# Performance work log

Measured on AMD Instinct MI355X. Metric: run time of the kernel, lower is better.

The kernel has to match this reference:

```python
import jax, jax.numpy as jnp
import numpy as np

EMBED_DIM = 1024
NUM_HEADS = 16
DEPTH = EMBED_DIM // NUM_HEADS
B, S = 4, 2048


def setup_inputs() -> dict:
    key = jax.random.key(0)
    ks = jax.random.split(key, 5)
    scale = 1.0 / np.sqrt(EMBED_DIM)
    return {
        "x": jax.random.normal(ks[0], (B, S, EMBED_DIM), dtype=jnp.float32),
        "wq_w": jax.random.normal(ks[1], (EMBED_DIM, EMBED_DIM), dtype=jnp.float32) * scale,
        "wq_b": jnp.zeros((EMBED_DIM,), dtype=jnp.float32),
        "wk_w": jax.random.normal(ks[2], (EMBED_DIM, EMBED_DIM), dtype=jnp.float32) * scale,
        "wk_b": jnp.zeros((EMBED_DIM,), dtype=jnp.float32),
        "wv_w": jax.random.normal(ks[3], (EMBED_DIM, EMBED_DIM), dtype=jnp.float32) * scale,
        "wv_b": jnp.zeros((EMBED_DIM,), dtype=jnp.float32),
        "wo_w": jax.random.normal(ks[4], (EMBED_DIM, EMBED_DIM), dtype=jnp.float32) * scale,
        "wo_b": jnp.zeros((EMBED_DIM,), dtype=jnp.float32),
    }


def _split_heads(t):
    # [B, S, E] -> [B, H, S, D]
    b, s, _ = t.shape
    return t.reshape(b, s, NUM_HEADS, DEPTH).transpose(0, 2, 1, 3)


def reference(x, wq_w, wq_b, wk_w, wk_b, wv_w, wv_b, wo_w, wo_b):
    q = _split_heads(x @ wq_w + wq_b)  # [B,H,S,D]
    k = _split_heads(x @ wk_w + wk_b)
    v = _split_heads(x @ wv_w + wv_b)

    scale = 1.0 / jnp.sqrt(jnp.asarray(DEPTH, dtype=x.dtype))
    scores = jnp.einsum("bhqd,bhkd->bhqk", q, k) * scale  # [B,H,S,S]

    s = x.shape[1]
    causal = jnp.tril(jnp.ones((s, s), dtype=x.dtype))  # 1 on/below diagonal
    scores = scores + (1.0 - causal)[None, None, :, :] * (-1e9)

    weights = jax.nn.softmax(scores, axis=-1)
    out = jnp.einsum("bhqk,bhkd->bhqd", weights, v)  # [B,H,S,D]
    out = out.transpose(0, 2, 1, 3).reshape(x.shape[0], s, EMBED_DIM)
    return out @ wo_w + wo_b
```

## Files before the change

kernel.cpp:

```cpp
#include <hip/hip_runtime.h>
#include <hip/hip_bf16.h>

#define E_DIM 1024
#define N_HEADS 16
#define HEAD_D 64
#define BATCH 4
#define SEQ 2048
#define M_ROWS (BATCH * SEQ)

typedef __attribute__((ext_vector_type(4))) float f32x4;
typedef __attribute__((ext_vector_type(8))) short s16x8;

__device__ __forceinline__ unsigned short f2b(float f) {
  union { float f; unsigned u; } v; v.f = f;
  unsigned r = v.u + 0x7fffu + ((v.u >> 16) & 1u);
  return (unsigned short)(r >> 16);
}

__device__ __forceinline__ unsigned packbf2(float lo, float hi) {
  union { __hip_bfloat162 h; unsigned u; } p;
  p.h = __float22bfloat162_rn(float2{lo, hi});
  return p.u;
}

__device__ __forceinline__ void gld16(const void* g, void* l) {
  __builtin_amdgcn_global_load_lds(
      (__attribute__((address_space(1))) void*)(g),
      (__attribute__((address_space(3))) void*)(l), 16, 0, 0);
}

__global__ __launch_bounds__(256) void cast_x_kernel(const float* __restrict__ in,
                                                     unsigned short* __restrict__ out,
                                                     int n4) {
  int i = blockIdx.x * 256 + threadIdx.x;
  const int stride = gridDim.x * 256;
  for (; i < n4; i += stride) {
    float4 v = ((const float4*)in)[i];
    ushort4 o;
    o.x = f2b(v.x); o.y = f2b(v.y); o.z = f2b(v.z); o.w = f2b(v.w);
    ((ushort4*)out)[i] = o;
  }
}

__global__ __launch_bounds__(256) void wtrans_kernel(const float* __restrict__ W,
                                                     unsigned short* __restrict__ WT) {
  __shared__ float t[64][65];
  const int k0 = blockIdx.x * 64, n0 = blockIdx.y * 64;
  const int tid = threadIdx.x;
  const int rr = tid >> 4, cc = (tid & 15) * 4;
  for (int p = 0; p < 4; ++p) {
    int row = p * 16 + rr;
    float4 v = *(const float4*)&W[(size_t)(k0 + row) * E_DIM + n0 + cc];
    t[row][cc] = v.x; t[row][cc + 1] = v.y; t[row][cc + 2] = v.z; t[row][cc + 3] = v.w;
  }
  __syncthreads();
  for (int p = 0; p < 4; ++p) {
    int nrow = p * 16 + rr;
    ushort4 o;
    o.x = f2b(t[cc][nrow]); o.y = f2b(t[cc + 1][nrow]);
    o.z = f2b(t[cc + 2][nrow]); o.w = f2b(t[cc + 3][nrow]);
    *(ushort4*)&WT[(size_t)(n0 + nrow) * E_DIM + k0 + cc] = o;
  }
}

__global__ __launch_bounds__(256) void gemm_qkv(const unsigned short* __restrict__ A,
                                                const unsigned short* __restrict__ BT,
                                                const float* __restrict__ bq,
                                                const float* __restrict__ bk,
                                                const float* __restrict__ bv,
                                                unsigned short* __restrict__ Qb,
                                                unsigned short* __restrict__ Kb,
                                                unsigned short* __restrict__ Vt) {
  __shared__ unsigned short Al[128 * 64];
  __shared__ unsigned short Bl[128 * 64];
  const int K = E_DIM;
  const int tid = threadIdx.x;
  const int lane = tid & 63;
  const int wave = tid >> 6;
  const int wr = wave >> 1, wc = wave & 1;
  const int m0 = blockIdx.x * 128, n0 = blockIdx.y * 128;

  f32x4 acc[4][4] = {};
  const int srow = tid >> 3;
  const int scol = (tid & 7) * 8;
  const int koff_base = (lane >> 4) * 8;
  const int lrow = lane & 15;

  for (int k0 = 0; k0 < K; k0 += 64) {
    for (int p = 0; p < 4; ++p) {
      int row = p * 32 + srow;
      gld16((const void*)(A + (size_t)(m0 + row) * K + k0 + scol),
            (void*)(Al + p * 2048 + wave * 512));
      gld16((const void*)(BT + (size_t)(n0 + row) * K + k0 + scol),
            (void*)(Bl + p * 2048 + wave * 512));
    }
    __syncthreads();
    for (int ks = 0; ks < 2; ++ks) {
      const int koff = ks * 32 + koff_base;
      s16x8 af[4], bf_[4];
      for (int i = 0; i < 4; ++i)
        af[i] = *(const s16x8*)&Al[(wr * 64 + i * 16 + lrow) * 64 + koff];
      for (int j = 0; j < 4; ++j)
        bf_[j] = *(const s16x8*)&Bl[(wc * 64 + j * 16 + lrow) * 64 + koff];
      for (int i = 0; i < 4; ++i)
        for (int j = 0; j < 4; ++j)
          acc[i][j] = __builtin_amdgcn_mfma_f32_16x16x32_bf16(af[i], bf_[j], acc[i][j], 0, 0, 0);
    }
    __syncthreads();
  }

  for (int j = 0; j < 4; ++j) {
    int c = n0 + wc * 64 + j * 16 + lrow;
    int proj = c >> 10, cc = c & 1023;
    float bvl = (proj == 0) ? bq[cc] : (proj == 1) ? bk[cc] : bv[cc];
    for (int i = 0; i < 4; ++i) {
      int r0 = m0 + wr * 64 + i * 16 + ((lane >> 4) << 2);
      for (int r = 0; r < 4; ++r) {
        float val = acc[i][j][r] + bvl;
        int m = r0 + r;
        if (proj == 0) {
          Qb[(size_t)m * E_DIM + cc] = f2b(val);
        } else if (proj == 1) {
          Kb[(size_t)m * E_DIM + cc] = f2b(val);
        } else {
          int b = m >> 11, s = m & 2047;
          int h = cc >> 6, d = cc & 63;
          Vt[((size_t)((b * 16 + h) * 64 + d)) * SEQ + s] = f2b(val);
        }
      }
    }
  }
}

__global__ __launch_bounds__(256) void gemm_out(const unsigned short* __restrict__ A,
                                                const unsigned short* __restrict__ BT,
                                                const float* __restrict__ bias,
                                                float* __restrict__ C) {
  __shared__ unsigned short Al[128 * 64];
  __shared__ unsigned short Bl[128 * 64];
  const int K = E_DIM, N = E_DIM;
  const int tid = threadIdx.x;
  const int lane = tid & 63;
  const int wave = tid >> 6;
  const int wr = wave >> 1, wc = wave & 1;
  const int m0 = blockIdx.x * 128, n0 = blockIdx.y * 128;

  f32x4 acc[4][4] = {};
  const int srow = tid >> 3;
  const int scol = (tid & 7) * 8;
  const int koff_base = (lane >> 4) * 8;
  const int lrow = lane & 15;

  for (int k0 = 0; k0 < K; k0 += 64) {
    for (int p = 0; p < 4; ++p) {
      int row = p * 32 + srow;
      gld16((const void*)(A + (size_t)(m0 + row) * K + k0 + scol),
            (void*)(Al + p * 2048 + wave * 512));
      gld16((const void*)(BT + (size_t)(n0 + row) * K + k0 + scol),
            (void*)(Bl + p * 2048 + wave * 512));
    }
    __syncthreads();
    for (int ks = 0; ks < 2; ++ks) {
      const int koff = ks * 32 + koff_base;
      s16x8 af[4], bf_[4];
      for (int i = 0; i < 4; ++i)
        af[i] = *(const s16x8*)&Al[(wr * 64 + i * 16 + lrow) * 64 + koff];
      for (int j = 0; j < 4; ++j)
        bf_[j] = *(const s16x8*)&Bl[(wc * 64 + j * 16 + lrow) * 64 + koff];
      for (int i = 0; i < 4; ++i)
        for (int j = 0; j < 4; ++j)
          acc[i][j] = __builtin_amdgcn_mfma_f32_16x16x32_bf16(af[i], bf_[j], acc[i][j], 0, 0, 0);
    }
    __syncthreads();
  }

  for (int j = 0; j < 4; ++j) {
    int col = n0 + wc * 64 + j * 16 + lrow;
    float bvl = bias[col];
    for (int i = 0; i < 4; ++i) {
      int r0 = m0 + wr * 64 + i * 16 + ((lane >> 4) << 2);
      for (int r = 0; r < 4; ++r)
        C[(size_t)(r0 + r) * N + col] = acc[i][j][r] + bvl;
    }
  }
}

__global__ __launch_bounds__(256, 2) void attn6_kernel(const unsigned short* __restrict__ Qb,
                                                       const unsigned short* __restrict__ Kb,
                                                       const unsigned short* __restrict__ Vt,
                                                       unsigned short* __restrict__ Ob) {
  __shared__ unsigned short Kl[2][4096];
  __shared__ unsigned short Vl[2][4096];

  const int tid = threadIdx.x, lane = tid & 63, wave = tid >> 6;
  const int id = blockIdx.x;
  const int xcd = id & 7;
  const int slot = id >> 3;
  const int bh = (xcd << 3) | (slot >> 4);
  const int ip = slot & 15;
  const size_t base = (size_t)(bh >> 4) * SEQ * E_DIM + (size_t)(bh & 15) * HEAD_D;
  const size_t baset = (size_t)bh * HEAD_D * SEQ;
  const int lq = lane & 15, lg = lane >> 4;

  const int row_lo = ip * 64 + wave * 16 + lq;
  const int row_hi = (31 - ip) * 64 + wave * 16 + lq;

  s16x8 qf0[2], qf1[2];
  {
    const unsigned short* p0 = Qb + base + (size_t)row_lo * E_DIM + lg * 8;
    qf0[0] = *(const s16x8*)p0; qf0[1] = *(const s16x8*)(p0 + 32);
    const unsigned short* p1 = Qb + base + (size_t)row_hi * E_DIM + lg * 8;
    qf1[0] = *(const s16x8*)p1; qf1[1] = *(const s16x8*)(p1 + 32);
  }

  const short onebf = (short)0x3F80;
  const s16x8 ones = {onebf, onebf, onebf, onebf, onebf, onebf, onebf, onebf};

  float m0r = -1e30f, m1r = -1e30f;
  f32x4 o0[4] = {}, o1[4] = {};
  f32x4 l0 = {}, l1 = {};
  const float scale2 = 0.125f * 1.44269504089f;
  const int ntm1 = 31 - ip;
  const bool hi5 = (lane & 32) != 0, hi4 = (lane & 16) != 0;

  const int o0b = tid << 4;
  const int o1b = 4096 + (tid << 4);
  const int r0s = o0b >> 7, r1s = o1b >> 7;
  const int c0s = ((o0b ^ ((r0s & 7) << 4)) & 127) >> 1;
  const int c1s = ((o1b ^ ((r1s & 7) << 4)) & 127) >> 1;
  const int dst0 = wave << 10;
  const int dst1 = 4096 + (wave << 10);

  auto stage = [&](int buf, int k0) {
    gld16((const void*)(Kb + base + (size_t)(k0 + r0s) * E_DIM + c0s),
          (void*)((char*)&Kl[buf][0] + dst0));
    gld16((const void*)(Kb + base + (size_t)(k0 + r1s) * E_DIM + c1s),
          (void*)((char*)&Kl[buf][0] + dst1));
    gld16((const void*)(Vt + baset + (size_t)r0s * SEQ + k0 + c0s),
          (void*)((char*)&Vl[buf][0] + dst0));
    gld16((const void*)(Vt + baset + (size_t)r1s * SEQ + k0 + c1s),
          (void*)((char*)&Vl[buf][0] + dst1));
  };

  const int swz = (lq & 7) << 4;

  auto process = [&](f32x4 (&sv)[4], int qrow, bool diag, float& mreg,
                     f32x4 (&oacc)[4], f32x4& lacc, int kk0, s16x8 (&vf)[4][2]) {
#pragma unroll
    for (int kb = 0; kb < 4; ++kb)
#pragma unroll
      for (int r = 0; r < 4; ++r) {
        float v = sv[kb][r] * scale2;
        if (diag) {
          int kk = kk0 + kb * 16 + lg * 4 + r;
          if (kk > qrow) v = -1e30f;
        }
        sv[kb][r] = v;
      }
    float mx = sv[0][0];
#pragma unroll
    for (int kb = 0; kb < 4; ++kb)
#pragma unroll
      for (int r = 0; r < 4; ++r) mx = fmaxf(mx, sv[kb][r]);
    mx = fmaxf(mx, __shfl_xor(mx, 16, 64));
    mx = fmaxf(mx, __shfl_xor(mx, 32, 64));
    float mn = fmaxf(mreg, mx);
    float corr = __builtin_amdgcn_exp2f(mreg - mn);
    mreg = mn;
    unsigned c[4][2];
#pragma unroll
    for (int kb = 0; kb < 4; ++kb)
#pragma unroll
      for (int rp = 0; rp < 2; ++rp) {
        float plo = __builtin_amdgcn_exp2f(sv[kb][2 * rp] - mn);
        float phi = __builtin_amdgcn_exp2f(sv[kb][2 * rp + 1] - mn);
        c[kb][rp] = packbf2(plo, phi);
      }
#pragma unroll
    for (int k1 = 0; k1 < 2; ++k1)
#pragma unroll
      for (int rp = 0; rp < 2; ++rp) {
        unsigned a = c[2 * k1][rp], b = c[2 * k1 + 1][rp];
        unsigned x = hi5 ? a : b;
        x = __shfl_xor(x, 32, 64);
        c[2 * k1][rp] = hi5 ? x : a;
        c[2 * k1 + 1][rp] = hi5 ? b : x;
      }
#pragma unroll
    for (int k1 = 0; k1 < 2; ++k1)
#pragma unroll
      for (int rp = 0; rp < 2; ++rp) {
        unsigned a = c[2 * k1][rp], b = c[2 * k1 + 1][rp];
        unsigned x = hi4 ? a : b;
        x = __shfl_xor(x, 16, 64);
        c[2 * k1][rp] = hi4 ? x : a;
        c[2 * k1 + 1][rp] = hi4 ? b : x;
      }
#pragma unroll
    for (int db = 0; db < 4; ++db) oacc[db] = oacc[db] * corr;
    lacc = lacc * corr;
#pragma unroll
    for (int ks = 0; ks < 2; ++ks) {
      union { unsigned w[4]; s16x8 v; } pu;
      pu.w[0] = c[2 * ks][0]; pu.w[1] = c[2 * ks][1];
      pu.w[2] = c[2 * ks + 1][0]; pu.w[3] = c[2 * ks + 1][1];
      lacc = __builtin_amdgcn_mfma_f32_16x16x32_bf16(ones, pu.v, lacc, 0, 0, 0);
#pragma unroll
      for (int db = 0; db < 4; ++db)
        oacc[db] = __builtin_amdgcn_mfma_f32_16x16x32_bf16(vf[db][ks], pu.v, oacc[db], 0, 0, 0);
    }
  };

  stage(0, 0);
  __syncthreads();
  int cur = 0;

  for (int t = 0; t <= ntm1; ++t) {
    if (t < ntm1) stage(cur ^ 1, (t + 1) * 64);

    const char* Kc = (const char*)&Kl[cur][0];
    const char* Vc = (const char*)&Vl[cur][0];
    s16x8 kf[4][2];
#pragma unroll
    for (int kb = 0; kb < 4; ++kb)
#pragma unroll
      for (int j = 0; j < 2; ++j)
        kf[kb][j] = *(const s16x8*)(Kc + (((kb * 16 + lq) * 128 + j * 64 + lg * 16) ^ swz));
    s16x8 vf[4][2];
#pragma unroll
    for (int db = 0; db < 4; ++db)
#pragma unroll
      for (int ks = 0; ks < 2; ++ks)
        vf[db][ks] = *(const s16x8*)(Vc + (((db * 16 + lq) * 128 + ks * 64 + lg * 16) ^ swz));

    const int kk0 = t * 64;
    {
      f32x4 s1v[4] = {};
#pragma unroll
      for (int kb = 0; kb < 4; ++kb) {
        s1v[kb] = __builtin_amdgcn_mfma_f32_16x16x32_bf16(kf[kb][0], qf1[0], s1v[kb], 0, 0, 0);
        s1v[kb] = __builtin_amdgcn_mfma_f32_16x16x32_bf16(kf[kb][1], qf1[1], s1v[kb], 0, 0, 0);
      }
      process(s1v, row_hi, t == ntm1, m1r, o1, l1, kk0, vf);
    }
    if (t <= ip) {
      f32x4 s0v[4] = {};
#pragma unroll
      for (int kb = 0; kb < 4; ++kb) {
        s0v[kb] = __builtin_amdgcn_mfma_f32_16x16x32_bf16(kf[kb][0], qf0[0], s0v[kb], 0, 0, 0);
        s0v[kb] = __builtin_amdgcn_mfma_f32_16x16x32_bf16(kf[kb][1], qf0[1], s0v[kb], 0, 0, 0);
      }
      process(s0v, row_lo, t == ip, m0r, o0, l0, kk0, vf);
    }

    __syncthreads();
    cur ^= 1;
  }

  {
    float inv0 = 1.0f / l0[0], inv1 = 1.0f / l1[0];
#pragma unroll
    for (int db = 0; db < 4; ++db) {
      ushort4 w0, w1;
      w0.x = f2b(o0[db][0] * inv0); w0.y = f2b(o0[db][1] * inv0);
      w0.z = f2b(o0[db][2] * inv0); w0.w = f2b(o0[db][3] * inv0);
      w1.x = f2b(o1[db][0] * inv1); w1.y = f2b(o1[db][1] * inv1);
      w1.z = f2b(o1[db][2] * inv1); w1.w = f2b(o1[db][3] * inv1);
      *(ushort4*)&Ob[base + (size_t)row_lo * E_DIM + db * 16 + lg * 4] = w0;
      *(ushort4*)&Ob[base + (size_t)row_hi * E_DIM + db * 16 + lg * 4] = w1;
    }
  }
}

extern "C" void kernel_launch(void* const* d_in, const int* in_sizes, int n_in,
                              void* d_out, int out_size, void* d_ws, size_t ws_size,
                              hipStream_t stream) {
  const float* x    = (const float*)d_in[0];
  const float* wq_w = (const float*)d_in[1];
  const float* wq_b = (const float*)d_in[2];
  const float* wk_w = (const float*)d_in[3];
  const float* wk_b = (const float*)d_in[4];
  const float* wv_w = (const float*)d_in[5];
  const float* wv_b = (const float*)d_in[6];
  const float* wo_w = (const float*)d_in[7];
  const float* wo_b = (const float*)d_in[8];
  float* out = (float*)d_out;

  const size_t XE = (size_t)M_ROWS * E_DIM;
  const size_t WE = (size_t)E_DIM * E_DIM;
  char* ws = (char*)d_ws;
  unsigned short* xb    = (unsigned short*)ws; ws += XE * 2;
  unsigned short* wqkvT = (unsigned short*)ws; ws += 3 * WE * 2;
  unsigned short* woT   = (unsigned short*)ws; ws += WE * 2;
  unsigned short* Qb    = (unsigned short*)ws; ws += XE * 2;
  unsigned short* Kb    = (unsigned short*)ws; ws += XE * 2;
  unsigned short* Vt    = (unsigned short*)ws; ws += XE * 2;
  unsigned short* Ao    = (unsigned short*)ws; ws += XE * 2;

  cast_x_kernel<<<2048, 256, 0, stream>>>(x, xb, (int)(XE / 4));
  dim3 tg(E_DIM / 64, E_DIM / 64);
  wtrans_kernel<<<tg, 256, 0, stream>>>(wq_w, wqkvT);
  wtrans_kernel<<<tg, 256, 0, stream>>>(wk_w, wqkvT + WE);
  wtrans_kernel<<<tg, 256, 0, stream>>>(wv_w, wqkvT + 2 * WE);
  wtrans_kernel<<<tg, 256, 0, stream>>>(wo_w, woT);

  gemm_qkv<<<dim3(M_ROWS / 128, 3072 / 128), 256, 0, stream>>>(
      xb, wqkvT, wq_b, wk_b, wv_b, Qb, Kb, Vt);

  attn6_kernel<<<1024, 256, 0, stream>>>(Qb, Kb, Vt, Ao);

  gemm_out<<<dim3(M_ROWS / 128, E_DIM / 128), 256, 0, stream>>>(Ao, woT, wo_b, out);
}
```

Baseline: 229.4 us.

## Double-buffer GEMM LDS tiles with XOR swizzle and batch weight transposes

```diff
diff --git a/kernel.cpp b/kernel.cpp
--- a/kernel.cpp
+++ b/kernel.cpp
@@ -42,8 +42,17 @@
   }
 }
 
-__global__ __launch_bounds__(256) void wtrans_kernel(const float* __restrict__ W,
-                                                     unsigned short* __restrict__ WT) {
+__global__ __launch_bounds__(256) void wtrans4_kernel(const float* __restrict__ W0,
+                                                      const float* __restrict__ W1,
+                                                      const float* __restrict__ W2,
+                                                      const float* __restrict__ W3,
+                                                      unsigned short* __restrict__ D0,
+                                                      unsigned short* __restrict__ D1,
+                                                      unsigned short* __restrict__ D2,
+                                                      unsigned short* __restrict__ D3) {
+  const int z = blockIdx.z;
+  const float* W = (z == 0) ? W0 : (z == 1) ? W1 : (z == 2) ? W2 : W3;
+  unsigned short* WT = (z == 0) ? D0 : (z == 1) ? D1 : (z == 2) ? D2 : D3;
   __shared__ float t[64][65];
   const int k0 = blockIdx.x * 64, n0 = blockIdx.y * 64;
   const int tid = threadIdx.x;
@@ -71,42 +80,67 @@
                                                 unsigned short* __restrict__ Qb,
                                                 unsigned short* __restrict__ Kb,
                                                 unsigned short* __restrict__ Vt) {
-  __shared__ unsigned short Al[128 * 64];
-  __shared__ unsigned short Bl[128 * 64];
+  __shared__ unsigned short Al[2][8192];
+  __shared__ unsigned short Bl[2][8192];
   const int K = E_DIM;
   const int tid = threadIdx.x;
   const int lane = tid & 63;
   const int wave = tid >> 6;
   const int wr = wave >> 1, wc = wave & 1;
   const int m0 = blockIdx.x * 128, n0 = blockIdx.y * 128;
+  const int lrow = lane & 15, lg = lane >> 4;
 
   f32x4 acc[4][4] = {};
-  const int srow = tid >> 3;
-  const int scol = (tid & 7) * 8;
-  const int koff_base = (lane >> 4) * 8;
-  const int lrow = lane & 15;
-
-  for (int k0 = 0; k0 < K; k0 += 64) {
+
+  const int ob = tid << 4;
+  const int dstb = (wave << 10);
+  int srow[4], scol[4];
+#pragma unroll
+  for (int p = 0; p < 4; ++p) {
+    int o = p * 4096 + ob;
+    srow[p] = o >> 7;
+    scol[p] = ((o ^ ((srow[p] & 7) << 4)) & 127) >> 1;
+  }
+
+  auto stage = [&](int buf, int k0) {
+#pragma unroll
     for (int p = 0; p < 4; ++p) {
-      int row = p * 32 + srow;
-      gld16((const void*)(A + (size_t)(m0 + row) * K + k0 + scol),
-            (void*)(Al + p * 2048 + wave * 512));
-      gld16((const void*)(BT + (size_t)(n0 + row) * K + k0 + scol),
-            (void*)(Bl + p * 2048 + wave * 512));
-    }
-    __syncthreads();
+      gld16((const void*)(A + (size_t)(m0 + srow[p]) * K + k0 + scol[p]),
+            (void*)((char*)&Al[buf][0] + p * 4096 + dstb));
+      gld16((const void*)(BT + (size_t)(n0 + srow[p]) * K + k0 + scol[p]),
+            (void*)((char*)&Bl[buf][0] + p * 4096 + dstb));
+    }
+  };
+
+  const int swz = (lrow & 7) << 4;
+
+  stage(0, 0);
+  __syncthreads();
+  int cur = 0;
+  const int nt = K / 64;
+
+  for (int t = 0; t < nt; ++t) {
+    if (t + 1 < nt) stage(cur ^ 1, (t + 1) * 64);
+    const char* Ac = (const char*)&Al[cur][0];
+    const char* Bc = (const char*)&Bl[cur][0];
+#pragma unroll
     for (int ks = 0; ks < 2; ++ks) {
-      const int koff = ks * 32 + koff_base;
+      const int cb = ks * 64 + lg * 16;
       s16x8 af[4], bf_[4];
+#pragma unroll
       for (int i = 0; i < 4; ++i)
-        af[i] = *(const s16x8*)&Al[(wr * 64 + i * 16 + lrow) * 64 + koff];
+        af[i] = *(const s16x8*)(Ac + (((wr * 64 + i * 16 + lrow) * 128 + cb) ^ swz));
+#pragma unroll
       for (int j = 0; j < 4; ++j)
-        bf_[j] = *(const s16x8*)&Bl[(wc * 64 + j * 16 + lrow) * 64 + koff];
+        bf_[j] = *(const s16x8*)(Bc + (((wc * 64 + j * 16 + lrow) * 128 + cb) ^ swz));
+#pragma unroll
       for (int i = 0; i < 4; ++i)
+#pragma unroll
         for (int j = 0; j < 4; ++j)
           acc[i][j] = __builtin_amdgcn_mfma_f32_16x16x32_bf16(af[i], bf_[j], acc[i][j], 0, 0, 0);
     }
     __syncthreads();
+    cur ^= 1;
   }
 
   for (int j = 0; j < 4; ++j) {
@@ -114,7 +148,7 @@
     int proj = c >> 10, cc = c & 1023;
     float bvl = (proj == 0) ? bq[cc] : (proj == 1) ? bk[cc] : bv[cc];
     for (int i = 0; i < 4; ++i) {
-      int r0 = m0 + wr * 64 + i * 16 + ((lane >> 4) << 2);
+      int r0 = m0 + wr * 64 + i * 16 + (lg << 2);
       for (int r = 0; r < 4; ++r) {
         float val = acc[i][j][r] + bvl;
         int m = r0 + r;
@@ -136,49 +170,74 @@
                                                 const unsigned short* __restrict__ BT,
                                                 const float* __restrict__ bias,
                                                 float* __restrict__ C) {
-  __shared__ unsigned short Al[128 * 64];
-  __shared__ unsigned short Bl[128 * 64];
+  __shared__ unsigned short Al[2][8192];
+  __shared__ unsigned short Bl[2][8192];
   const int K = E_DIM, N = E_DIM;
   const int tid = threadIdx.x;
   const int lane = tid & 63;
   const int wave = tid >> 6;
   const int wr = wave >> 1, wc = wave & 1;
   const int m0 = blockIdx.x * 128, n0 = blockIdx.y * 128;
+  const int lrow = lane & 15, lg = lane >> 4;
 
   f32x4 acc[4][4] = {};
-  const int srow = tid >> 3;
-  const int scol = (tid & 7) * 8;
-  const int koff_base = (lane >> 4) * 8;
-  const int lrow = lane & 15;
-
-  for (int k0 = 0; k0 < K; k0 += 64) {
+
+  const int ob = tid << 4;
+  const int dstb = (wave << 10);
+  int srow[4], scol[4];
+#pragma unroll
+  for (int p = 0; p < 4; ++p) {
+    int o = p * 4096 + ob;
+    srow[p] = o >> 7;
+    scol[p] = ((o ^ ((srow[p] & 7) << 4)) & 127) >> 1;
+  }
+
+  auto stage = [&](int buf, int k0) {
+#pragma unroll
     for (int p = 0; p < 4; ++p) {
-      int row = p * 32 + srow;
-      gld16((const void*)(A + (size_t)(m0 + row) * K + k0 + scol),
-            (void*)(Al + p * 2048 + wave * 512));
-      gld16((const void*)(BT + (size_t)(n0 + row) * K + k0 + scol),
-            (void*)(Bl + p * 2048 + wave * 512));
-    }
-    __syncthreads();
+      gld16((const void*)(A + (size_t)(m0 + srow[p]) * K + k0 + scol[p]),
+            (void*)((char*)&Al[buf][0] + p * 4096 + dstb));
+      gld16((const void*)(BT + (size_t)(n0 + srow[p]) * K + k0 + scol[p]),
+            (void*)((char*)&Bl[buf][0] + p * 4096 + dstb));
+    }
+  };
+
+  const int swz = (lrow & 7) << 4;
+
+  stage(0, 0);
+  __syncthreads();
+  int cur = 0;
+  const int nt = K / 64;
+
+  for (int t = 0; t < nt; ++t) {
+    if (t + 1 < nt) stage(cur ^ 1, (t + 1) * 64);
+    const char* Ac = (const char*)&Al[cur][0];
+    const char* Bc = (const char*)&Bl[cur][0];
+#pragma unroll
     for (int ks = 0; ks < 2; ++ks) {
-      const int koff = ks * 32 + koff_base;
+      const int cb = ks * 64 + lg * 16;
       s16x8 af[4], bf_[4];
+#pragma unroll
       for (int i = 0; i < 4; ++i)
-        af[i] = *(const s16x8*)&Al[(wr * 64 + i * 16 + lrow) * 64 + koff];
+        af[i] = *(const s16x8*)(Ac + (((wr * 64 + i * 16 + lrow) * 128 + cb) ^ swz));
+#pragma unroll
       for (int j = 0; j < 4; ++j)
-        bf_[j] = *(const s16x8*)&Bl[(wc * 64 + j * 16 + lrow) * 64 + koff];
+        bf_[j] = *(const s16x8*)(Bc + (((wc * 64 + j * 16 + lrow) * 128 + cb) ^ swz));
+#pragma unroll
       for (int i = 0; i < 4; ++i)
+#pragma unroll
         for (int j = 0; j < 4; ++j)
           acc[i][j] = __builtin_amdgcn_mfma_f32_16x16x32_bf16(af[i], bf_[j], acc[i][j], 0, 0, 0);
     }
     __syncthreads();
+    cur ^= 1;
   }
 
   for (int j = 0; j < 4; ++j) {
     int col = n0 + wc * 64 + j * 16 + lrow;
     float bvl = bias[col];
     for (int i = 0; i < 4; ++i) {
-      int r0 = m0 + wr * 64 + i * 16 + ((lane >> 4) << 2);
+      int r0 = m0 + wr * 64 + i * 16 + (lg << 2);
       for (int r = 0; r < 4; ++r)
         C[(size_t)(r0 + r) * N + col] = acc[i][j][r] + bvl;
     }
@@ -398,11 +457,8 @@
   unsigned short* Ao    = (unsigned short*)ws; ws += XE * 2;
 
   cast_x_kernel<<<2048, 256, 0, stream>>>(x, xb, (int)(XE / 4));
-  dim3 tg(E_DIM / 64, E_DIM / 64);
-  wtrans_kernel<<<tg, 256, 0, stream>>>(wq_w, wqkvT);
-  wtrans_kernel<<<tg, 256, 0, stream>>>(wk_w, wqkvT + WE);
-  wtrans_kernel<<<tg, 256, 0, stream>>>(wv_w, wqkvT + 2 * WE);
-  wtrans_kernel<<<tg, 256, 0, stream>>>(wo_w, woT);
+  wtrans4_kernel<<<dim3(E_DIM / 64, E_DIM / 64, 4), 256, 0, stream>>>(
+      wq_w, wk_w, wv_w, wo_w, wqkvT, wqkvT + WE, wqkvT + 2 * WE, woT);
 
   gemm_qkv<<<dim3(M_ROWS / 128, 3072 / 128), 256, 0, stream>>>(
       xb, wqkvT, wq_b, wk_b, wv_b, Qb, Kb, Vt);
```

Result: faster. 206.4 us (-10.0%).
